# Kernel optimization log

Measured on AMD Instinct MI355X. Metric: run time of the kernel, lower is better.

## Reference

```python
import jax, jax.numpy as jnp
import numpy as np

EPS = 1e-6
BN_EPS = 1e-5
STAGES = 10


def setup_inputs() -> dict:
    key = jax.random.key(0)
    ks = jax.random.split(key, 8)
    B, L, C, K, INNER = 16, 2048, 256, 64, 4096
    x = jax.random.normal(ks[0], (B, L, C), jnp.float32)
    group_tokens = jax.random.normal(ks[1], (B, K, C), jnp.float32)
    mu0 = jax.random.normal(ks[2], (1, K, C), jnp.float32) * np.sqrt(2.0 / C)
    mu0 = mu0 / (EPS + jnp.linalg.norm(mu0, axis=2, keepdims=True))
    w1 = jax.random.normal(ks[3], (INNER, C), jnp.float32) * 0.02
    b1 = jnp.zeros((INNER,), jnp.float32)
    gamma = jnp.ones((INNER,), jnp.float32)
    beta = jnp.zeros((INNER,), jnp.float32)
    bn_mean = jnp.zeros((INNER,), jnp.float32)
    bn_var = jnp.ones((INNER,), jnp.float32)
    w2 = jax.random.normal(ks[4], (C, INNER), jnp.float32) * 0.02
    b2 = jnp.zeros((C,), jnp.float32)
    return {"x": x, "group_tokens": group_tokens, "mu0": mu0, "w1": w1,
            "b1": b1, "gamma": gamma, "beta": beta, "bn_mean": bn_mean,
            "bn_var": bn_var, "w2": w2, "b2": b2}


def _em_loop(x, mu):
    # x: [B,L,C], mu: [B,K,C]; 10-step soft-clustering fixed point (no_grad in torch)
    def step(carry, _):
        mu, _ = carry
        z = jax.nn.softmax(jnp.einsum('blc,bkc->blk', x, mu), axis=-1)  # [B,L,K]
        z = z / (EPS + z.sum(axis=1, keepdims=True))
        mu = jnp.einsum('blk,blc->bkc', z, x)
        mu = mu / (EPS + jnp.linalg.norm(mu, axis=2, keepdims=True))
        return (mu, z), None
    z0 = jnp.zeros(x.shape[:2] + (mu.shape[1],), x.dtype)
    (mu, z), _ = jax.lax.scan(step, (mu, z0), None, length=STAGES)
    return jax.lax.stop_gradient(mu), jax.lax.stop_gradient(z)


def _project_mlp(x, w1, b1, gamma, beta, bn_mean, bn_var, w2, b2):
    # Conv1d(k=1) == channelwise linear; BN in eval mode with running stats
    h = jnp.einsum('blc,ic->bli', x, w1) + b1                 # [B,L,INNER]
    h = (h - bn_mean) * (gamma / jnp.sqrt(bn_var + BN_EPS)) + beta
    h = jax.nn.relu(h)
    return jnp.einsum('bli,oi->blo', h, w2) + b2              # [B,L,C]


def reference(x, group_tokens, mu0, w1, b1, gamma, beta, bn_mean, bn_var, w2, b2):
    B = group_tokens.shape[0]
    mu = jnp.broadcast_to(mu0, (B,) + mu0.shape[1:])
    mu, z = _em_loop(x, mu)
    recon_x = jnp.einsum('blk,bkc->blc', z, mu)
    recon_x = _project_mlp(recon_x, w1, b1, gamma, beta, bn_mean, bn_var, w2, b2)
    new_z = jax.nn.softmax(jnp.einsum('blc,bkc->blk', x, mu), axis=-1)
    attn_map = new_z / (EPS + new_z.sum(axis=1, keepdims=True))  # [B,L,K]
    attn_map = jnp.transpose(attn_map, (0, 2, 1))[:, None]       # [B,1,K,L]
    return mu, attn_map, recon_x
```

## Files before the change

### kernel.cpp

```cpp
#include <hip/hip_runtime.h>

constexpr int B_ = 16, L_ = 2048, C_ = 256, K_ = 64, INNER_ = 4096;
constexpr int NCH = 16;
constexpr int RPB = 128;
#define EPSF 1e-6f

typedef __attribute__((ext_vector_type(8)))  short bf16x8;
typedef __attribute__((ext_vector_type(4)))  float f32x4;
typedef __attribute__((ext_vector_type(16))) float f32x16;
typedef _Float16 f16;
typedef __attribute__((ext_vector_type(8))) _Float16 f16x8;
typedef __attribute__((ext_vector_type(4))) _Float16 f16x4;

__device__ __forceinline__ unsigned short f2bf(float f) {
  union { float f; unsigned u; } v; v.f = f;
  unsigned r = v.u + 0x7fffu + ((v.u >> 16) & 1u);
  return (unsigned short)(r >> 16);
}

__device__ __forceinline__ void gload16(const void* src, void* lds) {
  __builtin_amdgcn_global_load_lds(
      (const __attribute__((address_space(1))) unsigned*)src,
      (__attribute__((address_space(3))) unsigned*)lds, 16, 0, 0);
}

__global__ __launch_bounds__(256) void k_pre(
    const float* __restrict__ w1, const float* __restrict__ w2,
    const float* __restrict__ gamma, const float* __restrict__ beta,
    const float* __restrict__ bmean, const float* __restrict__ bvar,
    const float* __restrict__ b1, const float* __restrict__ mu0,
    unsigned short* __restrict__ w1bf, unsigned short* __restrict__ w2bf,
    f16* __restrict__ bnshH, f16* __restrict__ muF)
{
  int i = blockIdx.x * 256 + threadIdx.x;
  if (i < INNER_ * C_) {
    int r = i >> 8;
    float sc = gamma[r] * rsqrtf(bvar[r] + 1e-5f);
    w1bf[i] = f2bf(w1[i] * sc);
    w2bf[i] = f2bf(w2[i]);
  }
  if (i < B_ * K_ * C_) muF[i] = (f16)mu0[i & (K_ * C_ - 1)];
  if (i < INNER_) {
    float sc = gamma[i] * rsqrtf(bvar[i] + 1e-5f);
    bnshH[i] = (f16)fmaf(b1[i] - bmean[i], sc, beta[i]);
  }
}

__global__ __launch_bounds__(256) void k_xT(const float* __restrict__ x,
                                            f16* __restrict__ xf, f16* __restrict__ xTf)
{
  __shared__ float ts[64][65];
  int l0 = blockIdx.x * 64, c0 = blockIdx.y * 64, b = blockIdx.z;
  int t = threadIdx.x;
  for (int p = 0; p < 16; ++p) {
    int e = t + p * 256, i = e >> 6, j = e & 63;
    float vv = x[((size_t)b * L_ + l0 + i) * C_ + c0 + j];
    ts[i][j] = vv;
    xf[((size_t)b * L_ + l0 + i) * C_ + c0 + j] = (f16)vv;
  }
  __syncthreads();
  for (int p = 0; p < 16; ++p) {
    int e = t + p * 256, i = e >> 6, j = e & 63;
    xTf[((size_t)b * C_ + c0 + i) * L_ + l0 + j] = (f16)ts[j][i];
  }
}

template<bool DO_MU, bool WRITE_Z>
__global__ __launch_bounds__(512, 2) void k_em(
    const f16* __restrict__ xf,
    const f16* __restrict__ xTf,
    const f16* __restrict__ muF,
    f16* __restrict__ zout,
    float* __restrict__ cp,
    f16* __restrict__ part)
{
  __shared__ f16 mu_s[K_ * C_];
  __shared__ f16 zT_s[K_ * RPB];
  __shared__ f16 xtile[C_ * RPB];
  __shared__ float cpart[8][K_];

  int t = threadIdx.x, b = blockIdx.y, chn = blockIdx.x, l0 = chn * RPB;
  int w = t >> 6, lane = t & 63, l15 = lane & 15, g = lane >> 4;

#pragma unroll
  for (int q = 0; q < 4; ++q) {
    int s = q * 512 + t, k = s >> 5, sl = s & 31;
    gload16(muF + (size_t)b * (K_ * C_) + k * C_ + ((sl ^ (k & 15)) << 3), mu_s + s * 8);
  }
  __builtin_amdgcn_sched_barrier(0);
  f16x8 xfr[8];
  const f16* xr = xf + ((size_t)b * L_ + l0 + w * 16 + l15) * C_ + g * 8;
#pragma unroll
  for (int ck = 0; ck < 8; ++ck) xfr[ck] = *(const f16x8*)(xr + ck * 32);
  __builtin_amdgcn_sched_barrier(0);
  if (DO_MU) {
#pragma unroll
    for (int q = 0; q < 8; ++q) {
      int s = q * 512 + t, c = s >> 4, sl = s & 15;
      gload16(xTf + (size_t)(b * C_ + c) * L_ + l0 + ((sl ^ (c & 7)) << 3), xtile + s * 8);
    }
    __builtin_amdgcn_sched_barrier(0);
    asm volatile("s_waitcnt vmcnt(16)" ::: "memory");
  } else {
    asm volatile("s_waitcnt vmcnt(8)" ::: "memory");
  }
  __builtin_amdgcn_s_barrier();
  __builtin_amdgcn_sched_barrier(0);

  f32x4 acc[4];
#pragma unroll
  for (int mt = 0; mt < 4; ++mt)
#pragma unroll
    for (int j = 0; j < 4; ++j) acc[mt][j] = 0.f;
#pragma unroll
  for (int ck = 0; ck < 8; ++ck) {
#pragma unroll
    for (int mt = 0; mt < 4; ++mt) {
      f16x8 a = *(const f16x8*)(mu_s + (mt * 16 + l15) * C_ + (((ck * 4 + g) ^ l15) << 3));
      acc[mt] = __builtin_amdgcn_mfma_f32_16x16x32_f16(a, xfr[ck], acc[mt], 0, 0, 0);
    }
  }

  float z[4][4];
  {
    float mx = acc[0][0];
#pragma unroll
    for (int mt = 0; mt < 4; ++mt)
#pragma unroll
      for (int jj = 0; jj < 4; ++jj) mx = fmaxf(mx, acc[mt][jj]);
    mx = fmaxf(mx, __shfl_xor(mx, 16, 64));
    mx = fmaxf(mx, __shfl_xor(mx, 32, 64));
    float sm = 0.f;
#pragma unroll
    for (int mt = 0; mt < 4; ++mt)
#pragma unroll
      for (int jj = 0; jj < 4; ++jj) {
        float e = __expf(acc[mt][jj] - mx);
        z[mt][jj] = e; sm += e;
      }
    sm += __shfl_xor(sm, 16, 64);
    sm += __shfl_xor(sm, 32, 64);
    float inv = 1.f / sm;
#pragma unroll
    for (int mt = 0; mt < 4; ++mt)
#pragma unroll
      for (int jj = 0; jj < 4; ++jj) z[mt][jj] *= inv;
  }

#pragma unroll
  for (int mt = 0; mt < 4; ++mt)
#pragma unroll
    for (int jj = 0; jj < 4; ++jj) {
      float v = z[mt][jj];
      v += __shfl_xor(v, 1, 64); v += __shfl_xor(v, 2, 64);
      v += __shfl_xor(v, 4, 64); v += __shfl_xor(v, 8, 64);
      if (l15 == 0) cpart[w][mt * 16 + g * 4 + jj] = v;
    }

#pragma unroll
  for (int mt = 0; mt < 4; ++mt)
#pragma unroll
    for (int jj = 0; jj < 4; ++jj) {
      int k = mt * 16 + g * 4 + jj;
      int tl = w * 16 + l15;
      f16 h = (f16)z[mt][jj];
      if (DO_MU)   zT_s[k * RPB + (((tl >> 3) ^ (k & 15)) << 3) + (tl & 7)] = h;
      if (WRITE_Z) zout[((size_t)b * L_ + l0 + tl) * K_ + k] = h;
    }
  __syncthreads();

  if (t < K_) {
    float s = 0.f;
#pragma unroll
    for (int q = 0; q < 8; ++q) s += cpart[q][t];
    cp[(size_t)chn * (B_ * K_) + b * K_ + t] = s;
  }

  if (DO_MU) {
    f32x4 a3[4][2];
#pragma unroll
    for (int mt = 0; mt < 4; ++mt)
#pragma unroll
      for (int nt = 0; nt < 2; ++nt)
#pragma unroll
        for (int j = 0; j < 4; ++j) a3[mt][nt][j] = 0.f;
    int cb = w * 32;
#pragma unroll
    for (int ks = 0; ks < 4; ++ks) {
      f16x8 az[4], bx[2];
#pragma unroll
      for (int mt = 0; mt < 4; ++mt)
        az[mt] = *(const f16x8*)(zT_s + (mt * 16 + l15) * RPB + (((ks * 4 + g) ^ l15) << 3));
#pragma unroll
      for (int nt = 0; nt < 2; ++nt) {
        int c = cb + nt * 16 + l15;
        bx[nt] = *(const f16x8*)(xtile + c * RPB + (((ks * 4 + g) ^ (c & 7)) << 3));
      }
#pragma unroll
      for (int mt = 0; mt < 4; ++mt)
#pragma unroll
        for (int nt = 0; nt < 2; ++nt)
          a3[mt][nt] = __builtin_amdgcn_mfma_f32_16x16x32_f16(az[mt], bx[nt], a3[mt][nt], 0, 0, 0);
    }
    f16* pp = part + (((size_t)chn * B_ + b) * K_) * C_;
#pragma unroll
    for (int mt = 0; mt < 4; ++mt)
#pragma unroll
      for (int nt = 0; nt < 2; ++nt)
#pragma unroll
        for (int jj = 0; jj < 4; ++jj)
          pp[(size_t)(mt * 16 + g * 4 + jj) * C_ + cb + nt * 16 + l15] = (f16)a3[mt][nt][jj];
  }
}

template<bool LAST>
__global__ __launch_bounds__(256) void k_mufin(
    const f16* __restrict__ part, const float* __restrict__ cp,
    f16* __restrict__ muF, f16* __restrict__ muT,
    float* __restrict__ zsA, float* __restrict__ outmu)
{
  int b = blockIdx.x >> 4, kg = blockIdx.x & 15, t = threadIdx.x;
  int kr = t >> 6, c4 = t & 63, k = kg * 4 + kr;
  float a0 = 0.f, a1 = 0.f, a2 = 0.f, a3 = 0.f;
#pragma unroll
  for (int chn = 0; chn < NCH; ++chn) {
    f16x4 p = *(const f16x4*)(part + (((size_t)chn * B_ + b) * K_ + k) * C_ + c4 * 4);
    a0 += (float)p[0]; a1 += (float)p[1]; a2 += (float)p[2]; a3 += (float)p[3];
  }
  float zs = 0.f;
#pragma unroll
  for (int chn = 0; chn < NCH; ++chn) zs += cp[(size_t)chn * (B_ * K_) + b * K_ + k];
  float sc = 1.f / (EPSF + zs);
  a0 *= sc; a1 *= sc; a2 *= sc; a3 *= sc;
  float ssq = a0 * a0 + a1 * a1 + a2 * a2 + a3 * a3;
#pragma unroll
  for (int off = 32; off >= 1; off >>= 1) ssq += __shfl_xor(ssq, off, 64);
  float inv = 1.f / (EPSF + sqrtf(ssq));
  a0 *= inv; a1 *= inv; a2 *= inv; a3 *= inv;
  size_t base = (size_t)(b * K_ + k) * C_ + c4 * 4;
  f16x4 hm; hm[0] = (f16)a0; hm[1] = (f16)a1; hm[2] = (f16)a2; hm[3] = (f16)a3;
  *(f16x4*)(muF + base) = hm;
  if (c4 == 0) zsA[b * K_ + k] = zs;
  if (LAST) {
    *(float4*)(outmu + base) = make_float4(a0, a1, a2, a3);
    muT[((size_t)b * C_ + c4 * 4 + 0) * K_ + k] = hm[0];
    muT[((size_t)b * C_ + c4 * 4 + 1) * K_ + k] = hm[1];
    muT[((size_t)b * C_ + c4 * 4 + 2) * K_ + k] = hm[2];
    muT[((size_t)b * C_ + c4 * 4 + 3) * K_ + k] = hm[3];
  }
}

__global__ __launch_bounds__(256) void k_attn(
    const f16* __restrict__ zB, const float* __restrict__ cpB, float* __restrict__ attn)
{
  __shared__ float zt[64][68];
  __shared__ float inv_s[K_];
  int b = blockIdx.y, l0 = blockIdx.x * 64, t = threadIdx.x;
  if (t < K_) {
    float zs = 0.f;
#pragma unroll
    for (int chn = 0; chn < NCH; ++chn) zs += cpB[(size_t)chn * (B_ * K_) + b * K_ + t];
    inv_s[t] = 1.f / (EPSF + zs);
  }
  for (int p = 0; p < 16; ++p) {
    int e = t + p * 256, lo = e >> 6, k = e & 63;
    zt[lo][k] = (float)zB[((size_t)b * L_ + l0 + lo) * K_ + k];
  }
  __syncthreads();
  int lo = t & 63, kb = t >> 6;
  for (int p = 0; p < 16; ++p) {
    int k = kb * 16 + p;
    attn[((size_t)b * K_ + k) * L_ + l0 + lo] = zt[lo][k] * inv_s[k];
  }
}

__global__ __launch_bounds__(512, 2) void k_mlp(
    const f16* __restrict__ zA,
    const f16* __restrict__ muT,
    const float* __restrict__ zsA,
    const unsigned short* __restrict__ w1bf,
    const unsigned short* __restrict__ w2bf,
    const f16* __restrict__ bnshH, const float* __restrict__ b2,
    float* __restrict__ outr)
{
  __shared__ unsigned short w1s[2][64 * 256];
  __shared__ unsigned short w2s[2][256 * 64];
  __shared__ unsigned short hs[128 * 68];
  __shared__ f16 bns_s[INNER_];
  __shared__ float zinv_s[K_];

  int t = threadIdx.x, w = t >> 6, lane = t & 63, l31 = lane & 31, l5 = lane >> 5;
  int rb = blockIdx.x * 128, b = rb >> 11, l0 = rb & 2047;
  int tt = w >> 1, ih = w & 1;

  f16* muT_s = (f16*)w2s[0];
  f16* z_s   = (f16*)w2s[1];
  unsigned short* rcs = w1s[0];

  if (t < K_) zinv_s[t] = 1.f / (EPSF + zsA[b * K_ + t]);
#pragma unroll
  for (int q = 0; q < 4; ++q) {
    int s = q * 512 + t, c = s >> 3, sl = s & 7;
    gload16(muT + ((size_t)b * C_ + c) * K_ + ((sl ^ (c & 7)) << 3), muT_s + s * 8);
  }
#pragma unroll
  for (int q = 0; q < 2; ++q) {
    int s = q * 512 + t, tok = s >> 3, sl = s & 7;
    gload16(zA + ((size_t)b * L_ + l0 + tok) * K_ + ((sl ^ (tok & 7)) << 3), z_s + s * 8);
  }
  gload16(bnshH + t * 8, bns_s + t * 8);
  asm volatile("s_waitcnt vmcnt(0) lgkmcnt(0)" ::: "memory");
  __builtin_amdgcn_s_barrier();
  __builtin_amdgcn_sched_barrier(0);

  {
    f16x8 bz[4];
#pragma unroll
    for (int kk = 0; kk < 4; ++kk) {
      int tok = tt * 32 + l31;
      f16x8 zr = *(const f16x8*)(z_s + tok * 64 + (((kk * 2 + l5) ^ (tok & 7)) << 3));
      f16x8 sc;
#pragma unroll
      for (int e = 0; e < 8; ++e)
        sc[e] = (f16)((float)zr[e] * zinv_s[kk * 16 + l5 * 8 + e]);
      bz[kk] = sc;
    }
    f32x16 d0, d1, d2, d3;
#pragma unroll
    for (int r = 0; r < 16; ++r) { d0[r] = 0.f; d1[r] = 0.f; d2[r] = 0.f; d3[r] = 0.f; }
#pragma unroll
    for (int kk = 0; kk < 4; ++kk) {
#pragma unroll
      for (int m = 0; m < 4; ++m) {
        int c = ih * 128 + m * 32 + l31;
        f16x8 am = *(const f16x8*)(muT_s + c * 64 + (((kk * 2 + l5) ^ (c & 7)) << 3));
        if (m == 0) d0 = __builtin_amdgcn_mfma_f32_32x32x16_f16(am, bz[kk], d0, 0, 0, 0);
        if (m == 1) d1 = __builtin_amdgcn_mfma_f32_32x32x16_f16(am, bz[kk], d1, 0, 0, 0);
        if (m == 2) d2 = __builtin_amdgcn_mfma_f32_32x32x16_f16(am, bz[kk], d2, 0, 0, 0);
        if (m == 3) d3 = __builtin_amdgcn_mfma_f32_32x32x16_f16(am, bz[kk], d3, 0, 0, 0);
      }
    }
    asm volatile("s_waitcnt lgkmcnt(0)" ::: "memory");
    __builtin_amdgcn_s_barrier();
    __builtin_amdgcn_sched_barrier(0);
#pragma unroll
    for (int m = 0; m < 4; ++m) {
#pragma unroll
      for (int r = 0; r < 16; ++r) {
        int c = ih * 128 + m * 32 + (r & 3) + 8 * (r >> 2) + 4 * l5;
        int ks = c >> 4, l5p = (c >> 3) & 1, j = c & 7;
        float val = (m == 0) ? d0[r] : (m == 1) ? d1[r] : (m == 2) ? d2[r] : d3[r];
        rcs[(((tt * 16 + ks) * 64) + l5p * 32 + l31) * 8 + j] = f2bf(val);
      }
    }
  }
  asm volatile("s_waitcnt lgkmcnt(0)" ::: "memory");
  __builtin_amdgcn_s_barrier();
  __builtin_amdgcn_sched_barrier(0);

  bf16x8 rc[16];
#pragma unroll
  for (int ks = 0; ks < 16; ++ks)
    rc[ks] = *(const bf16x8*)(rcs + ((tt * 16 + ks) * 64 + lane) * 8);
  asm volatile("s_waitcnt lgkmcnt(0)" ::: "memory");
  __builtin_amdgcn_s_barrier();
  __builtin_amdgcn_sched_barrier(0);

  f32x16 acc2[4];
#pragma unroll
  for (int q = 0; q < 4; ++q)
#pragma unroll
    for (int r = 0; r < 16; ++r) acc2[q][r] = 0.f;

#define STAGE(ic, buf)                                                          \
  {                                                                             \
    _Pragma("unroll")                                                           \
    for (int q = 0; q < 4; ++q) {                                               \
      int d = q * 512 + t, i = d >> 5, sl = d & 31;                             \
      gload16(w1bf + (size_t)((ic) * 64 + i) * C_ + ((sl ^ (i & 15)) << 3),     \
              &w1s[buf][d * 8]);                                                \
    }                                                                           \
    _Pragma("unroll")                                                           \
    for (int q = 0; q < 4; ++q) {                                               \
      int d = q * 512 + t, o = d >> 3, sl = d & 7;                              \
      gload16(w2bf + (size_t)o * INNER_ + (ic) * 64 + ((sl ^ (o & 7)) << 3),    \
              &w2s[buf][d * 8]);                                                \
    }                                                                           \
  }

  STAGE(0, 0);
  for (int ic = 0; ic < 64; ++ic) {
    int cur = ic & 1;
    __builtin_amdgcn_sched_barrier(0);
    if (ic < 63) STAGE(ic + 1, cur ^ 1);
    __builtin_amdgcn_sched_barrier(0);
    if (ic < 63) { asm volatile("s_waitcnt vmcnt(8)" ::: "memory"); }
    else         { asm volatile("s_waitcnt vmcnt(0)" ::: "memory"); }
    __builtin_amdgcn_s_barrier();
    __builtin_amdgcn_sched_barrier(0);

    f32x16 h0, h1;
#pragma unroll
    for (int r = 0; r < 16; ++r) { h0[r] = 0.f; h1[r] = 0.f; }
    int irow = ih * 32 + l31;
#pragma unroll
    for (int ks = 0; ks < 16; ++ks) {
      bf16x8 a1 = *(const bf16x8*)(&w1s[cur][irow * 256 + (((ks * 2 + l5) ^ (irow & 15)) << 3)]);
      if (ks & 1) h1 = __builtin_amdgcn_mfma_f32_32x32x16_bf16(a1, rc[ks], h1, 0, 0, 0);
      else        h0 = __builtin_amdgcn_mfma_f32_32x32x16_bf16(a1, rc[ks], h0, 0, 0, 0);
    }
#pragma unroll
    for (int r = 0; r < 16; ++r) h0[r] += h1[r];

#pragma unroll
    for (int rp = 0; rp < 8; ++rp) {
      int r0 = rp * 2;
      int il = ih * 32 + 2 * (rp & 1) + 8 * (rp >> 1) + 4 * l5;
      float v0 = fmaxf(h0[r0]     + (float)bns_s[ic * 64 + il],     0.f);
      float v1 = fmaxf(h0[r0 + 1] + (float)bns_s[ic * 64 + il + 1], 0.f);
      unsigned u = (unsigned)f2bf(v0) | ((unsigned)f2bf(v1) << 16);
      *(unsigned*)(hs + (tt * 32 + l31) * 68 + il) = u;
    }
    asm volatile("s_waitcnt lgkmcnt(0)" ::: "memory");
    __builtin_amdgcn_s_barrier();
    __builtin_amdgcn_sched_barrier(0);

    __builtin_amdgcn_s_setprio(1);
#pragma unroll
    for (int ks2 = 0; ks2 < 4; ++ks2) {
      int orow = w * 32 + l31;
      bf16x8 a2 = *(const bf16x8*)(&w2s[cur][orow * 64 + (((ks2 * 2 + l5) ^ (orow & 7)) << 3)]);
#pragma unroll
      for (int t2 = 0; t2 < 4; ++t2) {
        bf16x8 bh = *(const bf16x8*)(&hs[(t2 * 32 + l31) * 68 + ks2 * 16 + l5 * 8]);
        acc2[t2] = __builtin_amdgcn_mfma_f32_32x32x16_bf16(a2, bh, acc2[t2], 0, 0, 0);
      }
    }
    __builtin_amdgcn_s_setprio(0);
    asm volatile("s_waitcnt lgkmcnt(0)" ::: "memory");
    __builtin_amdgcn_s_barrier();
    __builtin_amdgcn_sched_barrier(0);
  }
#undef STAGE

#pragma unroll
  for (int t2 = 0; t2 < 4; ++t2) {
    int tok = rb + t2 * 32 + l31;
#pragma unroll
    for (int q = 0; q < 4; ++q) {
      int o = w * 32 + q * 8 + l5 * 4;
      float4 bias = *(const float4*)(b2 + o);
      f32x4 v;
      v[0] = acc2[t2][q * 4 + 0] + bias.x;
      v[1] = acc2[t2][q * 4 + 1] + bias.y;
      v[2] = acc2[t2][q * 4 + 2] + bias.z;
      v[3] = acc2[t2][q * 4 + 3] + bias.w;
      *(f32x4*)(outr + (size_t)tok * C_ + o) = v;
    }
  }
}

extern "C" void kernel_launch(void* const* d_in, const int* in_sizes, int n_in,
                              void* d_out, int out_size, void* d_ws, size_t ws_size,
                              hipStream_t stream)
{
  const float* x     = (const float*)d_in[0];
  const float* mu0   = (const float*)d_in[2];
  const float* w1    = (const float*)d_in[3];
  const float* b1    = (const float*)d_in[4];
  const float* gamma = (const float*)d_in[5];
  const float* beta  = (const float*)d_in[6];
  const float* bmean = (const float*)d_in[7];
  const float* bvar  = (const float*)d_in[8];
  const float* w2    = (const float*)d_in[9];
  const float* b2    = (const float*)d_in[10];
  float* out = (float*)d_out;

  char* wsb = (char*)d_ws;
  f16* part = (f16*)(wsb + 0);
  f16* zB   = part;
  f16* zA   = (f16*)(wsb + 8388608);
  f16* xf   = (f16*)(wsb + 12582912);
  f16* xTf  = (f16*)(wsb + 29360128);
  unsigned short* w1bf = (unsigned short*)(wsb + 46137344);
  unsigned short* w2bf = (unsigned short*)(wsb + 48234496);
  f16*   muF   = (f16*)(wsb + 50331648);
  f16*   muT   = (f16*)(wsb + 50855936);
  f16*   bnshH = (f16*)(wsb + 51380224);
  float* cpA   = (float*)(wsb + 51388416);
  float* cpB   = (float*)(wsb + 51453952);
  float* zsA   = (float*)(wsb + 51519488);

  k_pre<<<4096, 256, 0, stream>>>(w1, w2, gamma, beta, bmean, bvar, b1, mu0,
                                  w1bf, w2bf, bnshH, muF);
  k_xT<<<dim3(32, 4, 16), 256, 0, stream>>>(x, xf, xTf);

  for (int s = 0; s < 10; ++s) {
    if (s == 9) k_em<true, true ><<<dim3(16, 16), 512, 0, stream>>>(xf, xTf, muF, zA, cpA, part);
    else        k_em<true, false><<<dim3(16, 16), 512, 0, stream>>>(xf, xTf, muF, zA, cpA, part);
    if (s == 9) k_mufin<true ><<<256, 256, 0, stream>>>(part, cpA, muF, muT, zsA, out);
    else        k_mufin<false><<<256, 256, 0, stream>>>(part, cpA, muF, muT, zsA, out);
  }
  k_em<false, true><<<dim3(16, 16), 512, 0, stream>>>(xf, xTf, muF, zB, cpB, part);
  k_attn<<<dim3(32, 16), 256, 0, stream>>>(zB, cpB, out + 262144);
  k_mlp<<<256, 512, 0, stream>>>(zA, muT, zsA, w1bf, w2bf, bnshH, b2, out + 2359296);
}
```

Measured before the change: 356.6 us.

## Load MLP w2 fragments directly into registers in pre-permuted MFMA order

The preprocessing kernel now writes w2 in bf16, permuted into the per-lane MFMA A-fragment order. k_mlp then loads each wave's w2 operands straight from global memory into registers each iteration, instead of staging w2 tiles through double-buffered LDS. This shrinks the shared-memory footprint into one aliased pool and removes the LDS writes and reads for w2. The per-iteration vmcnt wait moves to the trailing barrier, and the bias loads are vectorised. The cost is that w2 global-load latency now sits on each wave's register path, and every iteration waits for all outstanding loads at its end.

```diff
diff --git a/kernel.cpp b/kernel.cpp
--- a/kernel.cpp
+++ b/kernel.cpp
@@ -29,7 +29,7 @@
     const float* __restrict__ gamma, const float* __restrict__ beta,
     const float* __restrict__ bmean, const float* __restrict__ bvar,
     const float* __restrict__ b1, const float* __restrict__ mu0,
-    unsigned short* __restrict__ w1bf, unsigned short* __restrict__ w2bf,
+    unsigned short* __restrict__ w1bf, unsigned short* __restrict__ w2fr,
     f16* __restrict__ bnshH, f16* __restrict__ muF)
 {
   int i = blockIdx.x * 256 + threadIdx.x;
@@ -37,7 +37,10 @@
     int r = i >> 8;
     float sc = gamma[r] * rsqrtf(bvar[r] + 1e-5f);
     w1bf[i] = f2bf(w1[i] * sc);
-    w2bf[i] = f2bf(w2[i]);
+    int j = i & 7, l31 = (i >> 3) & 31, w = (i >> 8) & 7, l5 = (i >> 11) & 1, ks = i >> 12;
+    int ii = ks * 16 + l5 * 8 + j;
+    int o  = w * 32 + l31;
+    w2fr[i] = f2bf(w2[(size_t)o * INNER_ + ii]);
   }
   if (i < B_ * K_ * C_) muF[i] = (f16)mu0[i & (K_ * C_ - 1)];
   if (i < INNER_) {
@@ -274,29 +277,37 @@
   }
 }
 
+constexpr int W1S_OFF = 0;
+constexpr int HS_OFF  = 65536;
+constexpr int BNS_OFF = 83200;
+constexpr int MUT_OFF = 0;
+constexpr int ZS_OFF  = 32768;
+constexpr int RCS_OFF = 49152;
+constexpr int POOL_SZ = 114688;
+
 __global__ __launch_bounds__(512, 2) void k_mlp(
     const f16* __restrict__ zA,
     const f16* __restrict__ muT,
     const float* __restrict__ zsA,
     const unsigned short* __restrict__ w1bf,
-    const unsigned short* __restrict__ w2bf,
+    const unsigned short* __restrict__ w2fr,
     const f16* __restrict__ bnshH, const float* __restrict__ b2,
     float* __restrict__ outr)
 {
-  __shared__ unsigned short w1s[2][64 * 256];
-  __shared__ unsigned short w2s[2][256 * 64];
-  __shared__ unsigned short hs[128 * 68];
-  __shared__ f16 bns_s[INNER_];
+  __shared__ __align__(16) char pool[POOL_SZ];
   __shared__ float zinv_s[K_];
+
+  unsigned short* w1s = (unsigned short*)(pool + W1S_OFF);
+  unsigned short* hs  = (unsigned short*)(pool + HS_OFF);
+  f16* bns_s          = (f16*)(pool + BNS_OFF);
+  f16* muT_s          = (f16*)(pool + MUT_OFF);
+  f16* z_s            = (f16*)(pool + ZS_OFF);
+  unsigned short* rcs = (unsigned short*)(pool + RCS_OFF);
 
   int t = threadIdx.x, w = t >> 6, lane = t & 63, l31 = lane & 31, l5 = lane >> 5;
   int rb = blockIdx.x * 128, b = rb >> 11, l0 = rb & 2047;
   int tt = w >> 1, ih = w & 1;
 
-  f16* muT_s = (f16*)w2s[0];
-  f16* z_s   = (f16*)w2s[1];
-  unsigned short* rcs = w1s[0];
-
   if (t < K_) zinv_s[t] = 1.f / (EPSF + zsA[b * K_ + t]);
 #pragma unroll
   for (int q = 0; q < 4; ++q) {
@@ -308,7 +319,6 @@
     int s = q * 512 + t, tok = s >> 3, sl = s & 7;
     gload16(zA + ((size_t)b * L_ + l0 + tok) * K_ + ((sl ^ (tok & 7)) << 3), z_s + s * 8);
   }
-  gload16(bnshH + t * 8, bns_s + t * 8);
   asm volatile("s_waitcnt vmcnt(0) lgkmcnt(0)" ::: "memory");
   __builtin_amdgcn_s_barrier();
   __builtin_amdgcn_sched_barrier(0);
@@ -378,26 +388,29 @@
     for (int q = 0; q < 4; ++q) {                                               \
       int d = q * 512 + t, i = d >> 5, sl = d & 31;                             \
       gload16(w1bf + (size_t)((ic) * 64 + i) * C_ + ((sl ^ (i & 15)) << 3),     \
-              &w1s[buf][d * 8]);                                                \
+              w1s + (size_t)(buf) * 16384 + d * 8);                             \
     }                                                                           \
-    _Pragma("unroll")                                                           \
-    for (int q = 0; q < 4; ++q) {                                               \
-      int d = q * 512 + t, o = d >> 3, sl = d & 7;                              \
-      gload16(w2bf + (size_t)o * INNER_ + (ic) * 64 + ((sl ^ (o & 7)) << 3),    \
-              &w2s[buf][d * 8]);                                                \
-    }                                                                           \
-  }
-
+  }
+
+  gload16(bnshH + t * 8, bns_s + t * 8);
   STAGE(0, 0);
+  asm volatile("s_waitcnt vmcnt(0)" ::: "memory");
+  __builtin_amdgcn_s_barrier();
+  __builtin_amdgcn_sched_barrier(0);
+
+  const bf16x8* a2p = (const bf16x8*)w2fr;
+  int a2base = l5 * 256 + w * 32 + l31;
+
+#pragma unroll 2
   for (int ic = 0; ic < 64; ++ic) {
     int cur = ic & 1;
+    bf16x8 a2r[4];
+#pragma unroll
+    for (int ks2 = 0; ks2 < 4; ++ks2)
+      a2r[ks2] = a2p[(size_t)(ic * 4 + ks2) * 512 + a2base];
     __builtin_amdgcn_sched_barrier(0);
     if (ic < 63) STAGE(ic + 1, cur ^ 1);
     __builtin_amdgcn_sched_barrier(0);
-    if (ic < 63) { asm volatile("s_waitcnt vmcnt(8)" ::: "memory"); }
-    else         { asm volatile("s_waitcnt vmcnt(0)" ::: "memory"); }
-    __builtin_amdgcn_s_barrier();
-    __builtin_amdgcn_sched_barrier(0);
 
     f32x16 h0, h1;
 #pragma unroll
@@ -405,21 +418,31 @@
     int irow = ih * 32 + l31;
 #pragma unroll
     for (int ks = 0; ks < 16; ++ks) {
-      bf16x8 a1 = *(const bf16x8*)(&w1s[cur][irow * 256 + (((ks * 2 + l5) ^ (irow & 15)) << 3)]);
+      bf16x8 a1 = *(const bf16x8*)(w1s + cur * 16384 + irow * 256 +
+                                   (((ks * 2 + l5) ^ (irow & 15)) << 3));
       if (ks & 1) h1 = __builtin_amdgcn_mfma_f32_32x32x16_bf16(a1, rc[ks], h1, 0, 0, 0);
       else        h0 = __builtin_amdgcn_mfma_f32_32x32x16_bf16(a1, rc[ks], h0, 0, 0, 0);
     }
 #pragma unroll
     for (int r = 0; r < 16; ++r) h0[r] += h1[r];
 
-#pragma unroll
-    for (int rp = 0; rp < 8; ++rp) {
-      int r0 = rp * 2;
-      int il = ih * 32 + 2 * (rp & 1) + 8 * (rp >> 1) + 4 * l5;
-      float v0 = fmaxf(h0[r0]     + (float)bns_s[ic * 64 + il],     0.f);
-      float v1 = fmaxf(h0[r0 + 1] + (float)bns_s[ic * 64 + il + 1], 0.f);
-      unsigned u = (unsigned)f2bf(v0) | ((unsigned)f2bf(v1) << 16);
-      *(unsigned*)(hs + (tt * 32 + l31) * 68 + il) = u;
+    {
+      f16x4 bnv[4];
+#pragma unroll
+      for (int q = 0; q < 4; ++q)
+        bnv[q] = *(const f16x4*)(bns_s + ic * 64 + ih * 32 + q * 8 + l5 * 4);
+#pragma unroll
+      for (int q = 0; q < 4; ++q) {
+#pragma unroll
+        for (int pr = 0; pr < 2; ++pr) {
+          int r0 = q * 4 + pr * 2;
+          int il = ih * 32 + q * 8 + 4 * l5 + pr * 2;
+          float v0 = fmaxf(h0[r0]     + (float)bnv[q][pr * 2],     0.f);
+          float v1 = fmaxf(h0[r0 + 1] + (float)bnv[q][pr * 2 + 1], 0.f);
+          unsigned u = (unsigned)f2bf(v0) | ((unsigned)f2bf(v1) << 16);
+          *(unsigned*)(hs + (tt * 32 + l31) * 68 + il) = u;
+        }
+      }
     }
     asm volatile("s_waitcnt lgkmcnt(0)" ::: "memory");
     __builtin_amdgcn_s_barrier();
@@ -428,16 +451,14 @@
     __builtin_amdgcn_s_setprio(1);
 #pragma unroll
     for (int ks2 = 0; ks2 < 4; ++ks2) {
-      int orow = w * 32 + l31;
-      bf16x8 a2 = *(const bf16x8*)(&w2s[cur][orow * 64 + (((ks2 * 2 + l5) ^ (orow & 7)) << 3)]);
 #pragma unroll
       for (int t2 = 0; t2 < 4; ++t2) {
-        bf16x8 bh = *(const bf16x8*)(&hs[(t2 * 32 + l31) * 68 + ks2 * 16 + l5 * 8]);
-        acc2[t2] = __builtin_amdgcn_mfma_f32_32x32x16_bf16(a2, bh, acc2[t2], 0, 0, 0);
+        bf16x8 bh = *(const bf16x8*)(hs + (t2 * 32 + l31) * 68 + ks2 * 16 + l5 * 8);
+        acc2[t2] = __builtin_amdgcn_mfma_f32_32x32x16_bf16(a2r[ks2], bh, acc2[t2], 0, 0, 0);
       }
     }
     __builtin_amdgcn_s_setprio(0);
-    asm volatile("s_waitcnt lgkmcnt(0)" ::: "memory");
+    asm volatile("s_waitcnt vmcnt(0) lgkmcnt(0)" ::: "memory");
     __builtin_amdgcn_s_barrier();
     __builtin_amdgcn_sched_barrier(0);
   }
@@ -483,7 +504,7 @@
   f16* xf   = (f16*)(wsb + 12582912);
   f16* xTf  = (f16*)(wsb + 29360128);
   unsigned short* w1bf = (unsigned short*)(wsb + 46137344);
-  unsigned short* w2bf = (unsigned short*)(wsb + 48234496);
+  unsigned short* w2fr = (unsigned short*)(wsb + 48234496);
   f16*   muF   = (f16*)(wsb + 50331648);
   f16*   muT   = (f16*)(wsb + 50855936);
   f16*   bnshH = (f16*)(wsb + 51380224);
@@ -492,7 +513,7 @@
   float* zsA   = (float*)(wsb + 51519488);
 
   k_pre<<<4096, 256, 0, stream>>>(w1, w2, gamma, beta, bmean, bvar, b1, mu0,
-                                  w1bf, w2bf, bnshH, muF);
+                                  w1bf, w2fr, bnshH, muF);
   k_xT<<<dim3(32, 4, 16), 256, 0, stream>>>(x, xf, xTf);
 
   for (int s = 0; s < 10; ++s) {
@@ -503,5 +524,5 @@
   }
   k_em<false, true><<<dim3(16, 16), 512, 0, stream>>>(xf, xTf, muF, zB, cpB, part);
   k_attn<<<dim3(32, 16), 256, 0, stream>>>(zB, cpB, out + 262144);
-  k_mlp<<<256, 512, 0, stream>>>(zA, muT, zsA, w1bf, w2bf, bnshH, b2, out + 2359296);
-}
+  k_mlp<<<256, 512, 0, stream>>>(zA, muT, zsA, w1bf, w2fr, bnshH, b2, out + 2359296);
+}
```

After: 523.2 us. 46.7% more time.
